# Kernel optimization log

Measured on AMD Instinct MI355X. Metric: run time of the kernel, lower is better.

## Reference

```python
import jax, jax.numpy as jnp
import numpy as np

N_NODES = 20000
N_EDGES = 320000
IN_CH = 256
HID_CH = 256   # 2 * out_channels
OUT_CH = 128


def gcn_conv(x, edge_index, W, b, n_nodes):
    """PyG GCNConv: linear transform, add self-loops, sym-normalized scatter-add."""
    x = x @ W  # [N, C_out]
    loop = jnp.arange(n_nodes, dtype=edge_index.dtype)
    row = jnp.concatenate([edge_index[0], loop])  # source nodes
    col = jnp.concatenate([edge_index[1], loop])  # destination nodes
    deg = jax.ops.segment_sum(jnp.ones_like(col, dtype=x.dtype), col,
                              num_segments=n_nodes)
    deg_inv_sqrt = jnp.where(deg > 0, jax.lax.rsqrt(deg), 0.0)
    norm = deg_inv_sqrt[row] * deg_inv_sqrt[col]  # [E+N]
    msg = x[row] * norm[:, None]                  # gather + scale
    out = jax.ops.segment_sum(msg, col, num_segments=n_nodes)  # scatter-add
    return out + b


def setup_inputs() -> dict:
    key = jax.random.key(0)
    k1, k2, k3, k4, k5 = jax.random.split(key, 5)
    doc_embeds = jax.random.normal(k1, (N_NODES, IN_CH), dtype=jnp.float32)
    edge_index = jax.random.randint(k2, (2, N_EDGES), 0, N_NODES, dtype=jnp.int64)
    # Glorot-style init for GCN weights, zero bias (PyG defaults)
    s1 = 1.0 / np.sqrt(IN_CH)
    s2 = 1.0 / np.sqrt(HID_CH)
    W1 = jax.random.uniform(k3, (IN_CH, HID_CH), jnp.float32, -s1, s1)
    b1 = jnp.zeros((HID_CH,), jnp.float32)
    W2 = jax.random.uniform(k4, (HID_CH, OUT_CH), jnp.float32, -s2, s2)
    b2 = jnp.zeros((OUT_CH,), jnp.float32)
    return {"doc_embeds": doc_embeds, "edge_index": edge_index,
            "W1": W1, "b1": b1, "W2": W2, "b2": b2}


def reference(doc_embeds, edge_index, W1, b1, W2, b2):
    n = doc_embeds.shape[0]
    x = jax.nn.relu(gcn_conv(doc_embeds, edge_index, W1, b1, n))
    x = gcn_conv(x, edge_index, W2, b2, n)
    return x
```

## Files before the change

kernel.cpp:

```cpp
#include <hip/hip_runtime.h>
#include <math.h>

#define N_NODES 20000
#define N_EDGES 320000
#define IN_CH   256
#define HID_CH  256
#define OUT_CH  128
#define CAP     64
#define GK      256

typedef __attribute__((ext_vector_type(8))) short short8;
typedef __attribute__((ext_vector_type(8))) unsigned short ushort8;
typedef __attribute__((ext_vector_type(4))) unsigned short ushort4v;
typedef __attribute__((ext_vector_type(4))) float floatx4;
typedef __attribute__((ext_vector_type(2))) float floatx2;
typedef __attribute__((ext_vector_type(2))) _Float16 half2v;
typedef __attribute__((ext_vector_type(8))) _Float16 half8;

__global__ __launch_bounds__(256)
void prep_kernel(const float* __restrict__ W1, const float* __restrict__ W2,
                 _Float16* __restrict__ W1t, _Float16* __restrict__ W2t,
                 const int* __restrict__ row, const int* __restrict__ col,
                 int* __restrict__ deg, unsigned short* __restrict__ srcs) {
    const int g = blockIdx.x * blockDim.x + threadIdx.x;
    const int gsz = gridDim.x * blockDim.x;
    for (int t = g; t < (IN_CH * HID_CH) / 16; t += gsz) {
        int n = t >> 4;
        int kc = (t & 15) * 16;
        half8 h0, h1;
#pragma unroll
        for (int j = 0; j < 8; ++j) {
            h0[j] = (_Float16)W1[(size_t)(kc + j) * HID_CH + n];
            h1[j] = (_Float16)W1[(size_t)(kc + 8 + j) * HID_CH + n];
        }
        *(half8*)(W1t + (size_t)n * IN_CH + kc)     = h0;
        *(half8*)(W1t + (size_t)n * IN_CH + kc + 8) = h1;
    }
    for (int t = g; t < (HID_CH * OUT_CH) / 16; t += gsz) {
        int n = t >> 4;
        int kc = (t & 15) * 16;
        half8 h0, h1;
#pragma unroll
        for (int j = 0; j < 8; ++j) {
            h0[j] = (_Float16)W2[(size_t)(kc + j) * OUT_CH + n];
            h1[j] = (_Float16)W2[(size_t)(kc + 8 + j) * OUT_CH + n];
        }
        *(half8*)(W2t + (size_t)n * HID_CH + kc)     = h0;
        *(half8*)(W2t + (size_t)n * HID_CH + kc + 8) = h1;
    }
    for (int i = g; i < N_EDGES; i += gsz) {
        int c = col[i];
        int r = row[i];
        int p = atomicAdd(&deg[c], 1);
        srcs[(size_t)c * CAP + p] = (unsigned short)r;
    }
}

template <int AMODE, int TN>
__global__ __launch_bounds__(256, 2)
void gemm_mfma_kernel(const float* __restrict__ Afp, const _Float16* __restrict__ Ah,
                      const _Float16* __restrict__ Bt,
                      const int* __restrict__ deg, _Float16* __restrict__ C, int M, int N) {
    constexpr int NJ = TN / 32;
    __shared__ _Float16 As[64][36];
    __shared__ _Float16 Bs[TN][36];
    const int tid = threadIdx.x;
    const int m0 = blockIdx.y * 64;
    const int n0 = blockIdx.x * TN;
    const int lane = tid & 63;
    const int wave = tid >> 6;
    const int wr = (wave >> 1) * 32;
    const int wc = (wave & 1) * (TN / 2);
    const int lm = lane & 15;
    const int lk = (lane >> 4) * 8;

    floatx4 acc[2][NJ];
#pragma unroll
    for (int i = 0; i < 2; ++i)
#pragma unroll
        for (int j = 0; j < NJ; ++j) acc[i][j] = (floatx4){0.f, 0.f, 0.f, 0.f};

    const int ar  = tid >> 2;
    const int ako = (tid & 3) * 8;

    for (int k0 = 0; k0 < GK; k0 += 32) {
        {
            half8 va = {};
            if (m0 + ar < M) {
                if (AMODE == 1) {
                    const float* ap = Afp + (size_t)(m0 + ar) * GK + k0 + ako;
                    float4 f0 = *(const float4*)ap;
                    float4 f1 = *(const float4*)(ap + 4);
                    va[0] = (_Float16)f0.x; va[1] = (_Float16)f0.y;
                    va[2] = (_Float16)f0.z; va[3] = (_Float16)f0.w;
                    va[4] = (_Float16)f1.x; va[5] = (_Float16)f1.y;
                    va[6] = (_Float16)f1.z; va[7] = (_Float16)f1.w;
                } else {
                    va = *(const half8*)(Ah + (size_t)(m0 + ar) * GK + k0 + ako);
                }
            }
            *(half8*)&As[ar][ako] = va;
        }
#pragma unroll
        for (int c = 0; c < TN / 64; ++c) {
            int ch = tid + c * 256;
            int r  = ch >> 2;
            int ko = (ch & 3) * 8;
            *(half8*)&Bs[r][ko] = *(const half8*)(Bt + (size_t)(n0 + r) * GK + k0 + ko);
        }
        __syncthreads();

        half8 ah[2];
#pragma unroll
        for (int i = 0; i < 2; ++i)
            ah[i] = *(const half8*)&As[wr + i * 16 + lm][lk];
#pragma unroll
        for (int j = 0; j < NJ; ++j) {
            half8 bh = *(const half8*)&Bs[wc + j * 16 + lm][lk];
#pragma unroll
            for (int i = 0; i < 2; ++i)
                acc[i][j] = __builtin_amdgcn_mfma_f32_16x16x32_f16(ah[i], bh, acc[i][j], 0, 0, 0);
        }
        __syncthreads();
    }

#pragma unroll
    for (int i = 0; i < 2; ++i) {
#pragma unroll
        for (int r = 0; r < 4; ++r) {
            int rowi = m0 + wr + i * 16 + (lane >> 4) * 4 + r;
            if (rowi < M) {
                float dr = 1.0f / sqrtf((float)(deg[rowi] + 1));
#pragma unroll
                for (int j = 0; j < NJ; ++j) {
                    C[(size_t)rowi * N + n0 + wc + j * 16 + lm] = (_Float16)(dr * acc[i][j][r]);
                }
            }
        }
    }
}

template <int C, int NSLICE, int MODE>
__global__ __launch_bounds__(256)
void gather_sliced_kernel(const _Float16* __restrict__ X, const int* __restrict__ deg,
                          const unsigned short* __restrict__ srcs,
                          const float* __restrict__ bias, float* __restrict__ outf,
                          _Float16* __restrict__ outh, int n) {
    constexpr int SW = C / NSLICE;
    static_assert(SW == 32, "slice must be 32 channels");
    const int slice = blockIdx.x % NSLICE;
    const int ngrp  = blockIdx.x / NSLICE;
    const int wave = threadIdx.x >> 6;
    const int lane = threadIdx.x & 63;
    const int g  = lane >> 4;
    const int sl = lane & 15;
    const int node = ngrp * 16 + wave * 4 + g;
    if (node >= n) return;
    const int choff = slice * SW + sl * 2;
    const size_t beg = (size_t)node * CAP;
    const int cnt = deg[node];

    float a0 = 0.f, a1 = 0.f;
    int e = 0;
    for (; e + 4 <= cnt; e += 4) {
        ushort4v s4 = *(const ushort4v*)(srcs + beg + e);
        half2v v0 = *(const half2v*)(X + (size_t)s4.x * C + choff);
        half2v v1 = *(const half2v*)(X + (size_t)s4.y * C + choff);
        half2v v2 = *(const half2v*)(X + (size_t)s4.z * C + choff);
        half2v v3 = *(const half2v*)(X + (size_t)s4.w * C + choff);
        a0 += (float)v0.x + (float)v1.x + (float)v2.x + (float)v3.x;
        a1 += (float)v0.y + (float)v1.y + (float)v2.y + (float)v3.y;
    }
    for (; e < cnt; ++e) {
        int r = srcs[beg + e];
        half2v v = *(const half2v*)(X + (size_t)r * C + choff);
        a0 += (float)v.x; a1 += (float)v.y;
    }

    const float dc = 1.0f / sqrtf((float)(cnt + 1));
    half2v vsh = *(const half2v*)(X + (size_t)node * C + choff);
    float2 bb = *(const float2*)(bias + choff);

    float o0 = dc * (a0 + (float)vsh.x) + bb.x;
    float o1 = dc * (a1 + (float)vsh.y) + bb.y;

    if constexpr (MODE == 1) {
        half2v h;
        h.x = (_Float16)fmaxf(o0, 0.f);
        h.y = (_Float16)fmaxf(o1, 0.f);
        *(half2v*)(outh + (size_t)node * C + choff) = h;
    } else {
        floatx2 o = {o0, o1};
        __builtin_nontemporal_store(o, (floatx2*)(outf + (size_t)node * C + choff));
    }
}

extern "C" void kernel_launch(void* const* d_in, const int* in_sizes, int n_in,
                              void* d_out, int out_size, void* d_ws, size_t ws_size,
                              hipStream_t stream) {
    const float* doc_embeds = (const float*)d_in[0];
    const int*   edge_index = (const int*)d_in[1];
    const float* W1 = (const float*)d_in[2];
    const float* b1 = (const float*)d_in[3];
    const float* W2 = (const float*)d_in[4];
    const float* b2 = (const float*)d_in[5];
    float* out = (float*)d_out;

    const int* row = edge_index;
    const int* col = edge_index + N_EDGES;

    char* ws = (char*)d_ws;
    auto align_up = [](size_t x) { return (x + 255) / 256 * 256; };

    _Float16* X1s = (_Float16*)(ws);
    _Float16* H1  = (_Float16*)(ws + align_up((size_t)N_NODES * HID_CH * 2));
    _Float16* X2s = X1s;
    char* meta = (char*)(ws + 2 * align_up((size_t)N_NODES * HID_CH * 2));
    _Float16* W1t = (_Float16*)(meta); meta += align_up((size_t)IN_CH * HID_CH * 2);
    _Float16* W2t = (_Float16*)(meta); meta += align_up((size_t)HID_CH * OUT_CH * 2);
    int*            deg  = (int*)(meta);            meta += align_up((size_t)N_NODES * 4);
    unsigned short* srcs = (unsigned short*)(meta);

    hipMemsetAsync(deg, 0, (size_t)N_NODES * 4, stream);
    prep_kernel<<<(N_EDGES + 255) / 256, 256, 0, stream>>>(
        W1, W2, W1t, W2t, row, col, deg, srcs);

    {
        dim3 grid(HID_CH / 128, (N_NODES + 63) / 64);
        gemm_mfma_kernel<1, 128><<<grid, 256, 0, stream>>>(
            doc_embeds, nullptr, W1t, deg, X1s, N_NODES, HID_CH);
    }
    gather_sliced_kernel<HID_CH, 8, 1><<<((N_NODES + 15) / 16) * 8, 256, 0, stream>>>(
        X1s, deg, srcs, b1, nullptr, H1, N_NODES);

    {
        dim3 grid(OUT_CH / 128, (N_NODES + 63) / 64);
        gemm_mfma_kernel<2, 128><<<grid, 256, 0, stream>>>(
            nullptr, H1, W2t, deg, X2s, N_NODES, OUT_CH);
    }
    gather_sliced_kernel<OUT_CH, 4, 0><<<((N_NODES + 15) / 16) * 4, 256, 0, stream>>>(
        X2s, deg, srcs, b2, out, nullptr, N_NODES);
}
```

Measured before the change: 166.0 us.

## Overlap edge bucketing with first GEMM by moving degree norm into gather

The edge-bucketing pass (degree atomics and source lists) is split out of the prep kernel and run in the same launch as the first GEMM. Some blocks handle edges while the rest compute GEMM tiles, so the atomic scatter overlaps tensor work. To drop the GEMM's dependency on degrees, the source-side normalisation moves from the GEMM epilogue into the gather, which now reads deg[src] and computes an rsqrt per edge. The memset is folded into the prep kernel. The cost is extra per-edge degree loads and rsqrt work in both gather passes.

```diff
diff --git a/kernel.cpp b/kernel.cpp
--- a/kernel.cpp
+++ b/kernel.cpp
@@ -9,8 +9,9 @@
 #define CAP     64
 #define GK      256
 
-typedef __attribute__((ext_vector_type(8))) short short8;
-typedef __attribute__((ext_vector_type(8))) unsigned short ushort8;
+#define NEB      142
+#define G1_TILES 626
+
 typedef __attribute__((ext_vector_type(4))) unsigned short ushort4v;
 typedef __attribute__((ext_vector_type(4))) float floatx4;
 typedef __attribute__((ext_vector_type(2))) float floatx2;
@@ -18,12 +19,12 @@
 typedef __attribute__((ext_vector_type(8))) _Float16 half8;
 
 __global__ __launch_bounds__(256)
-void prep_kernel(const float* __restrict__ W1, const float* __restrict__ W2,
-                 _Float16* __restrict__ W1t, _Float16* __restrict__ W2t,
-                 const int* __restrict__ row, const int* __restrict__ col,
-                 int* __restrict__ deg, unsigned short* __restrict__ srcs) {
+void prep0_kernel(const float* __restrict__ W1, const float* __restrict__ W2,
+                  _Float16* __restrict__ W1t, _Float16* __restrict__ W2t,
+                  int* __restrict__ deg) {
     const int g = blockIdx.x * blockDim.x + threadIdx.x;
     const int gsz = gridDim.x * blockDim.x;
+    for (int i = g; i < N_NODES; i += gsz) deg[i] = 0;
     for (int t = g; t < (IN_CH * HID_CH) / 16; t += gsz) {
         int n = t >> 4;
         int kc = (t & 15) * 16;
@@ -48,25 +49,17 @@
         *(half8*)(W2t + (size_t)n * HID_CH + kc)     = h0;
         *(half8*)(W2t + (size_t)n * HID_CH + kc + 8) = h1;
     }
-    for (int i = g; i < N_EDGES; i += gsz) {
-        int c = col[i];
-        int r = row[i];
-        int p = atomicAdd(&deg[c], 1);
-        srcs[(size_t)c * CAP + p] = (unsigned short)r;
-    }
 }
 
 template <int AMODE, int TN>
-__global__ __launch_bounds__(256, 2)
-void gemm_mfma_kernel(const float* __restrict__ Afp, const _Float16* __restrict__ Ah,
-                      const _Float16* __restrict__ Bt,
-                      const int* __restrict__ deg, _Float16* __restrict__ C, int M, int N) {
+static __device__ __forceinline__ void gemm_tile(
+    const float* __restrict__ Afp, const _Float16* __restrict__ Ah,
+    const _Float16* __restrict__ Bt, _Float16* __restrict__ C,
+    int M, int N, int m0, int n0,
+    _Float16 (&As)[64][36], _Float16 (&Bs)[TN][36])
+{
     constexpr int NJ = TN / 32;
-    __shared__ _Float16 As[64][36];
-    __shared__ _Float16 Bs[TN][36];
     const int tid = threadIdx.x;
-    const int m0 = blockIdx.y * 64;
-    const int n0 = blockIdx.x * TN;
     const int lane = tid & 63;
     const int wave = tid >> 6;
     const int wr = (wave >> 1) * 32;
@@ -130,14 +123,44 @@
         for (int r = 0; r < 4; ++r) {
             int rowi = m0 + wr + i * 16 + (lane >> 4) * 4 + r;
             if (rowi < M) {
-                float dr = 1.0f / sqrtf((float)(deg[rowi] + 1));
 #pragma unroll
                 for (int j = 0; j < NJ; ++j) {
-                    C[(size_t)rowi * N + n0 + wc + j * 16 + lm] = (_Float16)(dr * acc[i][j][r]);
+                    C[(size_t)rowi * N + n0 + wc + j * 16 + lm] = (_Float16)acc[i][j][r];
                 }
             }
         }
     }
+}
+
+__global__ __launch_bounds__(256, 2)
+void gemm1_edge_kernel(const float* __restrict__ doc, const _Float16* __restrict__ W1t,
+                       const int* __restrict__ row, const int* __restrict__ col,
+                       int* __restrict__ deg, unsigned short* __restrict__ srcs,
+                       _Float16* __restrict__ X1s) {
+    __shared__ _Float16 As[64][36];
+    __shared__ _Float16 Bs[128][36];
+    const int bid = blockIdx.x;
+    if (bid < NEB) {
+        for (int i = bid * 256 + threadIdx.x; i < N_EDGES; i += NEB * 256) {
+            int c = col[i];
+            int r = row[i];
+            int p = atomicAdd(&deg[c], 1);
+            srcs[(size_t)c * CAP + p] = (unsigned short)r;
+        }
+    } else {
+        int t = bid - NEB;
+        gemm_tile<1, 128>(doc, nullptr, W1t, X1s, N_NODES, HID_CH,
+                          (t >> 1) * 64, (t & 1) * 128, As, Bs);
+    }
+}
+
+__global__ __launch_bounds__(256, 2)
+void gemm2_kernel(const _Float16* __restrict__ H1, const _Float16* __restrict__ W2t,
+                  _Float16* __restrict__ X2s) {
+    __shared__ _Float16 As[64][36];
+    __shared__ _Float16 Bs[128][36];
+    gemm_tile<2, 128>(nullptr, H1, W2t, X2s, N_NODES, OUT_CH,
+                      blockIdx.x * 64, 0, As, Bs);
 }
 
 template <int C, int NSLICE, int MODE>
@@ -164,25 +187,30 @@
     int e = 0;
     for (; e + 4 <= cnt; e += 4) {
         ushort4v s4 = *(const ushort4v*)(srcs + beg + e);
+        float w0 = 1.0f / sqrtf((float)(deg[s4.x] + 1));
+        float w1 = 1.0f / sqrtf((float)(deg[s4.y] + 1));
+        float w2 = 1.0f / sqrtf((float)(deg[s4.z] + 1));
+        float w3 = 1.0f / sqrtf((float)(deg[s4.w] + 1));
         half2v v0 = *(const half2v*)(X + (size_t)s4.x * C + choff);
         half2v v1 = *(const half2v*)(X + (size_t)s4.y * C + choff);
         half2v v2 = *(const half2v*)(X + (size_t)s4.z * C + choff);
         half2v v3 = *(const half2v*)(X + (size_t)s4.w * C + choff);
-        a0 += (float)v0.x + (float)v1.x + (float)v2.x + (float)v3.x;
-        a1 += (float)v0.y + (float)v1.y + (float)v2.y + (float)v3.y;
+        a0 += w0 * (float)v0.x + w1 * (float)v1.x + w2 * (float)v2.x + w3 * (float)v3.x;
+        a1 += w0 * (float)v0.y + w1 * (float)v1.y + w2 * (float)v2.y + w3 * (float)v3.y;
     }
     for (; e < cnt; ++e) {
         int r = srcs[beg + e];
+        float w = 1.0f / sqrtf((float)(deg[r] + 1));
         half2v v = *(const half2v*)(X + (size_t)r * C + choff);
-        a0 += (float)v.x; a1 += (float)v.y;
+        a0 += w * (float)v.x; a1 += w * (float)v.y;
     }
 
     const float dc = 1.0f / sqrtf((float)(cnt + 1));
     half2v vsh = *(const half2v*)(X + (size_t)node * C + choff);
     float2 bb = *(const float2*)(bias + choff);
 
-    float o0 = dc * (a0 + (float)vsh.x) + bb.x;
-    float o1 = dc * (a1 + (float)vsh.y) + bb.y;
+    float o0 = dc * (a0 + dc * (float)vsh.x) + bb.x;
+    float o1 = dc * (a1 + dc * (float)vsh.y) + bb.y;
 
     if constexpr (MODE == 1) {
         half2v h;
@@ -221,23 +249,16 @@
     int*            deg  = (int*)(meta);            meta += align_up((size_t)N_NODES * 4);
     unsigned short* srcs = (unsigned short*)(meta);
 
-    hipMemsetAsync(deg, 0, (size_t)N_NODES * 4, stream);
-    prep_kernel<<<(N_EDGES + 255) / 256, 256, 0, stream>>>(
-        W1, W2, W1t, W2t, row, col, deg, srcs);
-
-    {
-        dim3 grid(HID_CH / 128, (N_NODES + 63) / 64);
-        gemm_mfma_kernel<1, 128><<<grid, 256, 0, stream>>>(
-            doc_embeds, nullptr, W1t, deg, X1s, N_NODES, HID_CH);
-    }
+    prep0_kernel<<<256, 256, 0, stream>>>(W1, W2, W1t, W2t, deg);
+
+    gemm1_edge_kernel<<<NEB + G1_TILES, 256, 0, stream>>>(
+        doc_embeds, W1t, row, col, deg, srcs, X1s);
+
     gather_sliced_kernel<HID_CH, 8, 1><<<((N_NODES + 15) / 16) * 8, 256, 0, stream>>>(
         X1s, deg, srcs, b1, nullptr, H1, N_NODES);
 
-    {
-        dim3 grid(OUT_CH / 128, (N_NODES + 63) / 64);
-        gemm_mfma_kernel<2, 128><<<grid, 256, 0, stream>>>(
-            nullptr, H1, W2t, deg, X2s, N_NODES, OUT_CH);
-    }
+    gemm2_kernel<<<(N_NODES + 63) / 64, 256, 0, stream>>>(H1, W2t, X2s);
+
     gather_sliced_kernel<OUT_CH, 4, 0><<<((N_NODES + 15) / 16) * 4, 256, 0, stream>>>(
         X2s, deg, srcs, b2, out, nullptr, N_NODES);
 }
```

After: 217.0 us. 30.7% more time.
